# Optimization experiments

Hardware: AMD Instinct MI355X
Metric: run time of the kernel (lower is better)

## Reference

```python
import jax, jax.numpy as jnp
import numpy as np
import math

N = 12288
D = 64
SCALE0 = math.log(10.0)


def lorentz_linear(x, W, b, scale):
    # x: [N, D] -> nn.Linear then Lorentz re-normalization onto the hyperboloid
    h = x @ W.T + b
    time = jax.nn.sigmoid(h[:, :1]) * jnp.exp(scale) + 1.1  # [N, 1]
    xn = h[:, 1:]  # spatial components [N, D-1]
    sq = jnp.clip(jnp.sum(xn * xn, axis=-1, keepdims=True), 1e-8, None)
    s = (time * time - 1.0) / sq
    return jnp.concatenate([time, xn * jnp.sqrt(s)], axis=-1)


def setup_inputs() -> dict:
    key = jax.random.key(0)
    ks = jax.random.split(key, 8)
    stdv = 1.0 / math.sqrt(D)
    x = jax.random.normal(ks[0], (N, D), dtype=jnp.float32)
    # sparse-ish binary adjacency stored dense (module calls adj.to_dense())
    adj = (jax.random.uniform(ks[1], (N, N)) < 0.002).astype(jnp.float32)
    W = jax.random.uniform(ks[2], (D, D), minval=-stdv, maxval=stdv, dtype=jnp.float32)
    Wq = jax.random.uniform(ks[3], (D, D), minval=-stdv, maxval=stdv, dtype=jnp.float32)
    Wk = jax.random.uniform(ks[4], (D, D), minval=-stdv, maxval=stdv, dtype=jnp.float32)
    z = jnp.zeros((D,), dtype=jnp.float32)
    sc = jnp.asarray(SCALE0, dtype=jnp.float32)
    return {
        'x': x, 'adj': adj,
        'W': W, 'b': z, 'scale': sc,
        'Wq': Wq, 'bq': z, 'scale_q': sc,
        'Wk': Wk, 'bk': z, 'scale_k': sc,
        'att_bias': jnp.asarray(20.0, dtype=jnp.float32),
        'att_scale': jnp.asarray(math.sqrt(D), dtype=jnp.float32),
    }


def reference(x, adj, W, b, scale, Wq, bq, scale_q, Wk, bk, scale_k, att_bias, att_scale):
    # LorentzLinear
    h = lorentz_linear(x, W, b, scale)  # [N, D]
    # LorentzAgg with attention
    q = lorentz_linear(h, Wq, bq, scale_q)
    k = lorentz_linear(h, Wk, bk, scale_k)
    # cinner: Lorentzian inner product matrix (negate time component of q)
    qm = jnp.concatenate([-q[:, :1], q[:, 1:]], axis=-1)
    att = 2.0 + 2.0 * (qm @ k.T)                 # [N, N]
    att = jax.nn.sigmoid(att / att_scale + att_bias)
    att = adj * att                               # mask by adjacency
    support = att @ h                             # [N, D]
    # Lorentz self-inner: inner(v,v) = -v0^2 + sum(v_rest^2); denorm = sqrt(|-inner|)
    inner = -support[:, :1] ** 2 + jnp.sum(support[:, 1:] ** 2, axis=-1, keepdims=True)
    denorm = jnp.sqrt(jnp.clip(jnp.abs(-inner), 1e-8, None))
    return support / denorm
```

## Files before the change

kernel.cpp:

```cpp
#include <hip/hip_runtime.h>
#include <math.h>

#define N   12288
#define D   64
#define CAP 96

typedef unsigned int uint4n __attribute__((ext_vector_type(4)));

__device__ __forceinline__ float wave_sum(float v) {
    #pragma unroll
    for (int m = 32; m >= 1; m >>= 1) v += __shfl_xor(v, m, 64);
    return v;
}
__device__ __forceinline__ float sigmoidf(float a) { return 1.0f / (1.0f + __expf(-a)); }

__global__ __launch_bounds__(256) void linear_kernel(
        const float* __restrict__ x,
        const float* __restrict__ W,  const float* __restrict__ b,  const float* __restrict__ scale,
        const float* __restrict__ Wq, const float* __restrict__ bq, const float* __restrict__ scale_q,
        const float* __restrict__ Wk, const float* __restrict__ bk, const float* __restrict__ scale_k,
        float* __restrict__ h, float* __restrict__ qm, float* __restrict__ kmat) {
    __shared__ float Wl [D * (D + 1)];
    __shared__ float Wql[D * (D + 1)];
    __shared__ float Wkl[D * (D + 1)];

    const int tid  = threadIdx.x;
    const int lane = tid & 63;
    const int w    = tid >> 6;
    const int row  = blockIdx.x * 4 + w;

    for (int idx = tid; idx < D * D; idx += 256) {
        int d = idx >> 6, kk = idx & 63;
        Wl [d * (D + 1) + kk] = W [idx];
        Wql[d * (D + 1) + kk] = Wq[idx];
        Wkl[d * (D + 1) + kk] = Wk[idx];
    }
    __syncthreads();

    float hvv;
    {
        float xv  = x[row * D + lane];
        float acc = b[lane];
        const float* wr = &Wl[lane * (D + 1)];
        #pragma unroll
        for (int kk = 0; kk < D; ++kk)
            acc = fmaf(__shfl(xv, kk, 64), wr[kk], acc);
        float h0   = __shfl(acc, 0, 64);
        float time = __expf(scale[0]) * sigmoidf(h0) + 1.1f;
        float sq   = fmaxf(wave_sum((lane == 0) ? 0.0f : acc * acc), 1e-8f);
        float r    = sqrtf((time * time - 1.0f) / sq);
        hvv = (lane == 0) ? time : acc * r;
        h[row * D + lane] = hvv;
    }

    {
        float accq = bq[lane], acck = bk[lane];
        const float* wq = &Wql[lane * (D + 1)];
        const float* wk = &Wkl[lane * (D + 1)];
        #pragma unroll
        for (int kk = 0; kk < D; ++kk) {
            float xk = __shfl(hvv, kk, 64);
            accq = fmaf(xk, wq[kk], accq);
            acck = fmaf(xk, wk[kk], acck);
        }
        {
            float h0   = __shfl(accq, 0, 64);
            float time = __expf(scale_q[0]) * sigmoidf(h0) + 1.1f;
            float sq   = fmaxf(wave_sum((lane == 0) ? 0.0f : accq * accq), 1e-8f);
            float r    = sqrtf((time * time - 1.0f) / sq);
            qm[row * D + lane] = (lane == 0) ? -time : accq * r;
        }
        {
            float h0   = __shfl(acck, 0, 64);
            float time = __expf(scale_k[0]) * sigmoidf(h0) + 1.1f;
            float sq   = fmaxf(wave_sum((lane == 0) ? 0.0f : acck * acck), 1e-8f);
            float r    = sqrtf((time * time - 1.0f) / sq);
            kmat[row * D + lane] = (lane == 0) ? time : acck * r;
        }
    }
}

__global__ __launch_bounds__(256) void adj_gather_kernel(
        const uint4n* __restrict__ adj4,
        const float* __restrict__ qm,
        const float* __restrict__ kmat,
        const float* __restrict__ h,
        const float* __restrict__ att_bias_p,
        const float* __restrict__ att_scale_p,
        float* __restrict__ out) {
    __shared__ int scols[CAP];
    __shared__ int scnt;
    __shared__ float sacc[4][D];

    int tid  = threadIdx.x;
    int row  = blockIdx.x;
    if (tid == 0) scnt = 0;
    __syncthreads();

    const uint4n* rowp = adj4 + (size_t)row * (N / 4);
    #pragma unroll
    for (int it = 0; it < (N / 4) / 256; ++it) {
        int t = it * 256 + tid;
        uint4n v = __builtin_nontemporal_load(&rowp[t]);
        if ((v.x | v.y | v.z | v.w) != 0u) {
            unsigned e[4] = {v.x, v.y, v.z, v.w};
            #pragma unroll
            for (int c = 0; c < 4; ++c) {
                if (e[c] != 0u) {
                    int pos = atomicAdd(&scnt, 1);
                    if (pos < CAP) scols[pos] = t * 4 + c;
                }
            }
        }
    }
    __syncthreads();

    int m = scnt; if (m > CAP) m = CAP;
    int lane = tid & 63;
    int w    = tid >> 6;

    float qv        = qm[row * D + lane];
    float bias      = att_bias_p[0];
    float inv_scale = 1.0f / att_scale_p[0];

    float acc = 0.0f;
    for (int n = w; n < m; n += 4) {
        int j = scols[n];
        float dot = wave_sum(qv * kmat[j * D + lane]);
        float att = sigmoidf(fmaf(2.0f + 2.0f * dot, inv_scale, bias));
        acc = fmaf(att, h[j * D + lane], acc);
    }
    sacc[w][lane] = acc;
    __syncthreads();

    if (w == 0) {
        float total = sacc[0][lane] + sacc[1][lane] + sacc[2][lane] + sacc[3][lane];
        float contrib = (lane == 0) ? -total * total : total * total;
        float inner   = wave_sum(contrib);
        float denorm  = sqrtf(fmaxf(fabsf(inner), 1e-8f));
        out[row * D + lane] = total / denorm;
    }
}

extern "C" void kernel_launch(void* const* d_in, const int* in_sizes, int n_in,
                              void* d_out, int out_size, void* d_ws, size_t ws_size,
                              hipStream_t stream) {
    const float*  x         = (const float*)d_in[0];
    const uint4n* adj       = (const uint4n*)d_in[1];
    const float*  W         = (const float*)d_in[2];
    const float*  b         = (const float*)d_in[3];
    const float*  scale     = (const float*)d_in[4];
    const float*  Wq        = (const float*)d_in[5];
    const float*  bq        = (const float*)d_in[6];
    const float*  scale_q   = (const float*)d_in[7];
    const float*  Wk        = (const float*)d_in[8];
    const float*  bk        = (const float*)d_in[9];
    const float*  scale_k   = (const float*)d_in[10];
    const float*  att_bias  = (const float*)d_in[11];
    const float*  att_scale = (const float*)d_in[12];
    float* out = (float*)d_out;

    float* h    = (float*)d_ws;
    float* qm   = h  + (size_t)N * D;
    float* kmat = qm + (size_t)N * D;

    linear_kernel<<<N / 4, 256, 0, stream>>>(x, W, b, scale,
                                             Wq, bq, scale_q, Wk, bk, scale_k,
                                             h, qm, kmat);
    adj_gather_kernel<<<N, 256, 0, stream>>>(adj, qm, kmat, h,
                                             att_bias, att_scale, out);
}
```

Before: 800.0 us.

## Batch adjacency loads in halves, amortize weight staging over more rows

The linear kernel now processes 16 rows per block instead of 4, so the three weight matrices are staged into shared memory once per 16 rows and the scale exponentials are hoisted out of the row loop. The gather kernel issues six nontemporal 16-byte adjacency loads per thread before testing any of them, in two halves, to increase memory-level parallelism on the dense 600MB adjacency scan. It also hoists the q load above the first barrier, adds an occupancy hint of 8 blocks per CU, and unrolls the neighbor loop by 2. The cost is more registers held per thread and fewer blocks in the linear kernel.

```diff
diff --git a/kernel.cpp b/kernel.cpp
--- a/kernel.cpp
+++ b/kernel.cpp
@@ -1,9 +1,12 @@
 #include <hip/hip_runtime.h>
 #include <math.h>
 
-#define N   12288
-#define D   64
-#define CAP 96
+#define N    12288
+#define D    64
+#define CAP  96
+#define ITS  ((N / 4) / 256)
+#define HALF (ITS / 2)
+#define RPB  16
 
 typedef unsigned int uint4n __attribute__((ext_vector_type(4)));
 
@@ -27,7 +30,6 @@
     const int tid  = threadIdx.x;
     const int lane = tid & 63;
     const int w    = tid >> 6;
-    const int row  = blockIdx.x * 4 + w;
 
     for (int idx = tid; idx < D * D; idx += 256) {
         int d = idx >> 6, kk = idx & 63;
@@ -37,50 +39,58 @@
     }
     __syncthreads();
 
-    float hvv;
-    {
-        float xv  = x[row * D + lane];
-        float acc = b[lane];
-        const float* wr = &Wl[lane * (D + 1)];
-        #pragma unroll
-        for (int kk = 0; kk < D; ++kk)
-            acc = fmaf(__shfl(xv, kk, 64), wr[kk], acc);
-        float h0   = __shfl(acc, 0, 64);
-        float time = __expf(scale[0]) * sigmoidf(h0) + 1.1f;
-        float sq   = fmaxf(wave_sum((lane == 0) ? 0.0f : acc * acc), 1e-8f);
-        float r    = sqrtf((time * time - 1.0f) / sq);
-        hvv = (lane == 0) ? time : acc * r;
-        h[row * D + lane] = hvv;
-    }
+    const float* wr = &Wl [lane * (D + 1)];
+    const float* wq = &Wql[lane * (D + 1)];
+    const float* wk = &Wkl[lane * (D + 1)];
+    const float es  = __expf(scale[0]);
+    const float esq = __expf(scale_q[0]);
+    const float esk = __expf(scale_k[0]);
 
-    {
-        float accq = bq[lane], acck = bk[lane];
-        const float* wq = &Wql[lane * (D + 1)];
-        const float* wk = &Wkl[lane * (D + 1)];
-        #pragma unroll
-        for (int kk = 0; kk < D; ++kk) {
-            float xk = __shfl(hvv, kk, 64);
-            accq = fmaf(xk, wq[kk], accq);
-            acck = fmaf(xk, wk[kk], acck);
+    #pragma unroll
+    for (int s = 0; s < RPB / 4; ++s) {
+        const int row = blockIdx.x * RPB + s * 4 + w;
+
+        float hvv;
+        {
+            float xv  = x[row * D + lane];
+            float acc = b[lane];
+            #pragma unroll
+            for (int kk = 0; kk < D; ++kk)
+                acc = fmaf(__shfl(xv, kk, 64), wr[kk], acc);
+            float h0   = __shfl(acc, 0, 64);
+            float time = es * sigmoidf(h0) + 1.1f;
+            float sq   = fmaxf(wave_sum((lane == 0) ? 0.0f : acc * acc), 1e-8f);
+            float r    = sqrtf((time * time - 1.0f) / sq);
+            hvv = (lane == 0) ? time : acc * r;
+            h[row * D + lane] = hvv;
         }
         {
-            float h0   = __shfl(accq, 0, 64);
-            float time = __expf(scale_q[0]) * sigmoidf(h0) + 1.1f;
-            float sq   = fmaxf(wave_sum((lane == 0) ? 0.0f : accq * accq), 1e-8f);
-            float r    = sqrtf((time * time - 1.0f) / sq);
-            qm[row * D + lane] = (lane == 0) ? -time : accq * r;
-        }
-        {
-            float h0   = __shfl(acck, 0, 64);
-            float time = __expf(scale_k[0]) * sigmoidf(h0) + 1.1f;
-            float sq   = fmaxf(wave_sum((lane == 0) ? 0.0f : acck * acck), 1e-8f);
-            float r    = sqrtf((time * time - 1.0f) / sq);
-            kmat[row * D + lane] = (lane == 0) ? time : acck * r;
+            float accq = bq[lane], acck = bk[lane];
+            #pragma unroll
+            for (int kk = 0; kk < D; ++kk) {
+                float xk = __shfl(hvv, kk, 64);
+                accq = fmaf(xk, wq[kk], accq);
+                acck = fmaf(xk, wk[kk], acck);
+            }
+            {
+                float h0   = __shfl(accq, 0, 64);
+                float time = esq * sigmoidf(h0) + 1.1f;
+                float sq   = fmaxf(wave_sum((lane == 0) ? 0.0f : accq * accq), 1e-8f);
+                float r    = sqrtf((time * time - 1.0f) / sq);
+                qm[row * D + lane] = (lane == 0) ? -time : accq * r;
+            }
+            {
+                float h0   = __shfl(acck, 0, 64);
+                float time = esk * sigmoidf(h0) + 1.1f;
+                float sq   = fmaxf(wave_sum((lane == 0) ? 0.0f : acck * acck), 1e-8f);
+                float r    = sqrtf((time * time - 1.0f) / sq);
+                kmat[row * D + lane] = (lane == 0) ? time : acck * r;
+            }
         }
     }
 }
 
-__global__ __launch_bounds__(256) void adj_gather_kernel(
+__global__ __launch_bounds__(256, 8) void adj_gather_kernel(
         const uint4n* __restrict__ adj4,
         const float* __restrict__ qm,
         const float* __restrict__ kmat,
@@ -94,21 +104,32 @@
 
     int tid  = threadIdx.x;
     int row  = blockIdx.x;
+    int lane = tid & 63;
+    int w    = tid >> 6;
     if (tid == 0) scnt = 0;
+
+    const uint4n* rowp = adj4 + (size_t)row * (N / 4);
+    float qv = qm[row * D + lane];
     __syncthreads();
 
-    const uint4n* rowp = adj4 + (size_t)row * (N / 4);
-    #pragma unroll
-    for (int it = 0; it < (N / 4) / 256; ++it) {
-        int t = it * 256 + tid;
-        uint4n v = __builtin_nontemporal_load(&rowp[t]);
-        if ((v.x | v.y | v.z | v.w) != 0u) {
-            unsigned e[4] = {v.x, v.y, v.z, v.w};
-            #pragma unroll
-            for (int c = 0; c < 4; ++c) {
-                if (e[c] != 0u) {
-                    int pos = atomicAdd(&scnt, 1);
-                    if (pos < CAP) scols[pos] = t * 4 + c;
+    #pragma unroll 1
+    for (int half = 0; half < 2; ++half) {
+        uint4n v[HALF];
+        #pragma unroll
+        for (int i = 0; i < HALF; ++i)
+            v[i] = __builtin_nontemporal_load(&rowp[(half * HALF + i) * 256 + tid]);
+        #pragma unroll
+        for (int i = 0; i < HALF; ++i) {
+            uint4n u = v[i];
+            if ((u.x | u.y | u.z | u.w) != 0u) {
+                int t = (half * HALF + i) * 256 + tid;
+                unsigned e[4] = {u.x, u.y, u.z, u.w};
+                #pragma unroll
+                for (int c = 0; c < 4; ++c) {
+                    if (e[c] != 0u) {
+                        int pos = atomicAdd(&scnt, 1);
+                        if (pos < CAP) scols[pos] = t * 4 + c;
+                    }
                 }
             }
         }
@@ -116,14 +137,11 @@
     __syncthreads();
 
     int m = scnt; if (m > CAP) m = CAP;
-    int lane = tid & 63;
-    int w    = tid >> 6;
-
-    float qv        = qm[row * D + lane];
     float bias      = att_bias_p[0];
     float inv_scale = 1.0f / att_scale_p[0];
 
     float acc = 0.0f;
+    #pragma unroll 2
     for (int n = w; n < m; n += 4) {
         int j = scols[n];
         float dot = wave_sum(qv * kmat[j * D + lane]);
@@ -164,9 +182,9 @@
     float* qm   = h  + (size_t)N * D;
     float* kmat = qm + (size_t)N * D;
 
-    linear_kernel<<<N / 4, 256, 0, stream>>>(x, W, b, scale,
-                                             Wq, bq, scale_q, Wk, bk, scale_k,
-                                             h, qm, kmat);
+    linear_kernel<<<N / RPB, 256, 0, stream>>>(x, W, b, scale,
+                                               Wq, bq, scale_q, Wk, bk, scale_k,
+                                               h, qm, kmat);
     adj_gather_kernel<<<N, 256, 0, stream>>>(adj, qm, kmat, h,
                                              att_bias, att_scale, out);
 }
```

Result: no change. 813.7 us (+1.7%).
